# Kernel optimization log

Hardware: AMD Instinct MI355X
Metric: run time of the kernel (lower is better)

The kernel has to match this reference:

```python
import jax, jax.numpy as jnp
import numpy as np

H = 8          # num_heads
NUM_SEEDS = 4  # num_seeds (T = T0 + NUM_SEEDS in training/non_trivial)
NEG_INF = float('-inf')


def setup_inputs() -> dict:
    key = jax.random.key(0)
    ks = jax.random.split(key, 9)
    B, T, L, C = 4, 16, 64, 512
    T0 = T - NUM_SEEDS
    x = jax.random.normal(ks[0], (B, T0 * L, C), dtype=jnp.float32)
    x_ctx = jax.random.normal(ks[1], (B, T, L, C), dtype=jnp.float32)
    dx_ctx = jax.random.normal(ks[2], (B, T, L, C), dtype=jnp.float32)
    ctx_mask = jax.random.randint(ks[3], (B, T), 0, 2).astype(jnp.bool_)
    s = 1.0 / np.sqrt(C)
    qkv_w = jax.random.normal(ks[4], (3 * C, C), dtype=jnp.float32) * s
    k_w = jax.random.normal(ks[5], (C, C), dtype=jnp.float32) * s
    v_w = jax.random.normal(ks[6], (C, C), dtype=jnp.float32) * s
    proj_w = jax.random.normal(ks[7], (C, C), dtype=jnp.float32) * s
    proj_b = jax.random.normal(ks[8], (C,), dtype=jnp.float32) * 0.01
    return {"x": x, "x_ctx": x_ctx, "dx_ctx": dx_ctx, "ctx_mask": ctx_mask,
            "qkv_w": qkv_w, "k_w": k_w, "v_w": v_w, "proj_w": proj_w,
            "proj_b": proj_b}


def reference(x, x_ctx, dx_ctx, ctx_mask, qkv_w, k_w, v_w, proj_w, proj_b):
    B, T, L, C = x_ctx.shape
    T0 = x.shape[1] // L
    hd = C // H
    scale = hd ** (-0.5)

    # qkv for the current (self) tokens: [3, B, H, T0*L, hd]
    qkv = (x @ qkv_w.T).reshape(B, T0 * L, 3, H, hd).transpose(2, 0, 3, 1, 4)
    q, k, v = qkv[0], qkv[1], qkv[2]

    # context keys/values: [B, H, T*L, hd]
    k_ctx = (dx_ctx.reshape(B, T * L, C) @ k_w.T).reshape(B, T * L, H, hd).transpose(0, 2, 1, 3)
    v_ctx = (x_ctx.reshape(B, T * L, C) @ v_w.T).reshape(B, T * L, H, hd).transpose(0, 2, 1, 3)

    # cross-context scores: [B, H, T0*L, T, L]
    attn = (jnp.einsum('bhqd,bhkd->bhqk', q, k_ctx) * scale).reshape(B, H, T0 * L, T, L)

    # context mask: drop whole context frames where ctx_mask is False
    attn = jnp.where(ctx_mask[:, None, None, :, None], attn, NEG_INF)

    # non-trivial temporal mask (training): query frame i can't attend to
    # context frame i + num_seeds
    nt = (jnp.arange(T0)[:, None] + NUM_SEEDS) == jnp.arange(T)[None, :]  # [T0, T]
    attn6 = attn.reshape(B, H, T0, L, T, L)
    attn6 = jnp.where(nt[None, None, :, None, :, None], NEG_INF, attn6)
    attn = attn6.reshape(B, H, T0 * L, T, L)

    # per-frame self attention scores: [B, H, T0, L, L] -> [B, H, T0*L, 1, L]
    q6 = q.reshape(B, H, T0, L, hd)
    k6 = k.reshape(B, H, T0, L, hd)
    self_attn = (jnp.einsum('bhtqd,bhtkd->bhtqk', q6, k6) * scale).reshape(B, H, T0 * L, 1, L)

    # joint softmax over (T+1)*L keys
    attn = jnp.concatenate([attn, self_attn], axis=-2).reshape(B, H, T0 * L, (T + 1) * L)
    attn = jax.nn.softmax(attn, axis=-1)

    # split back: cross part @ v_ctx, self part @ v (per frame)
    out = jnp.einsum('bhqk,bhkd->bhqd', attn[:, :, :, :-L], v_ctx)
    a_self = attn[:, :, :, -L:].reshape(B, H, T0, L, L)
    v6 = v.reshape(B, H, T0, L, hd)
    out = out + jnp.einsum('bhtqk,bhtkd->bhtqd', a_self, v6).reshape(B, H, T0 * L, hd)

    out = out.transpose(0, 2, 1, 3).reshape(B, T0 * L, C)
    return out @ proj_w.T + proj_b
```

## Files before the change

### kernel.cpp

```cpp
#include <hip/hip_runtime.h>
#include <hip/hip_bf16.h>

typedef __attribute__((ext_vector_type(8))) short bf16x8;
typedef __attribute__((ext_vector_type(4))) float f32x4;

#define BB 4
#define TT 16
#define NT0 12
#define LL 64
#define CC 512
#define HH 8
#define HD 64
#define NQ (NT0*LL)
#define NCTX (TT*LL)

#define GPTR(x) ((__attribute__((address_space(1))) void*)(x))
#define SPTR(x) ((__attribute__((address_space(3))) void*)(x))
#define VMCNT(n) (((n) & 15) | (7u << 4) | (0xFu << 8))

__device__ __forceinline__ float bf2f(ushort u) {
  union { unsigned int i; float f; } x; x.i = ((unsigned int)u) << 16; return x.f;
}
__device__ __forceinline__ ushort f2bf(float f) {
  union { float f; unsigned int i; } x; x.f = f;
  unsigned int r = x.i + 0x7fffu + ((x.i >> 16) & 1u);
  return (ushort)(r >> 16);
}

__global__ __launch_bounds__(256) void cvt_all(const float* __restrict__ w0,
                                               const float* __restrict__ w1,
                                               const float* __restrict__ w2,
                                               const float* __restrict__ w3,
                                               const float* __restrict__ x,
                                               const float* __restrict__ xc,
                                               const float* __restrict__ dxc,
                                               ushort* __restrict__ dst) {
  long i = (long)blockIdx.x * 256 + threadIdx.x;
  const float* src; long off;
  if (i < 196608)       { src = w0;  off = 0; }
  else if (i < 262144)  { src = w1;  off = 196608; }
  else if (i < 327680)  { src = w2;  off = 262144; }
  else if (i < 393216)  { src = w3;  off = 327680; }
  else if (i < 786432)  { src = x;   off = 393216; }
  else if (i < 1310720) { src = xc;  off = 786432; }
  else                  { src = dxc; off = 1310720; }
  f32x4 v = *(const f32x4*)(src + (i - off) * 4);
  ushort4 o = { f2bf(v[0]), f2bf(v[1]), f2bf(v[2]), f2bf(v[3]) };
  *(ushort4*)(dst + i * 4) = o;
}

template<int MT>
__device__ __forceinline__ void gemm_mac(const ushort* __restrict__ A,
                                         const ushort* __restrict__ W,
                                         int mt, int nt, ushort* lds,
                                         f32x4* acc) {
  constexpr int ASZ = MT * 32;
  constexpr int BUF = ASZ + 4096;
  constexpr int L   = (MT == 128) ? 4 : 3;

  int t = threadIdx.x;
  int pa0 = t, pa1 = t + 256;
  int ra0 = pa0 >> 2, ra1 = pa1 >> 2;
  int ca0 = (pa0 & 3) ^ ((ra0 >> 1) & 3);
  int ca1 = (pa1 & 3) ^ ((ra1 >> 1) & 3);
  const ushort* ga0 = A + (size_t)(mt * MT + ra0) * 512 + ca0 * 8;
  const ushort* ga1 = A + (size_t)(mt * MT + ra1) * 512 + ca1 * 8;
  const ushort* gw0 = W + (size_t)(nt * 128 + ra0) * 512 + ca0 * 8;
  const ushort* gw1 = W + (size_t)(nt * 128 + ra1) * 512 + ca1 * 8;

  int lane = t & 63, l15 = lane & 15, kg = lane >> 4;
  int wv = t >> 6;
  int mh = (wv >> 1) * (MT / 2), nh = (wv & 1) * 64;
  int swz = kg ^ ((l15 >> 1) & 3);
  int faoff = (mh + l15) * 32 + swz * 8;
  int fwoff = (nh + l15) * 32 + swz * 8;

  auto stage = [&](int ks, int bb) {
    int ko = ks * 32;
    __builtin_amdgcn_global_load_lds(GPTR(ga0 + ko), SPTR(lds + bb + pa0 * 8), 16, 0, 0);
    if (MT == 128)
      __builtin_amdgcn_global_load_lds(GPTR(ga1 + ko), SPTR(lds + bb + pa1 * 8), 16, 0, 0);
    __builtin_amdgcn_global_load_lds(GPTR(gw0 + ko), SPTR(lds + bb + ASZ + pa0 * 8), 16, 0, 0);
    __builtin_amdgcn_global_load_lds(GPTR(gw1 + ko), SPTR(lds + bb + ASZ + pa1 * 8), 16, 0, 0);
  };

  stage(0, 0);
  stage(1, BUF);

#pragma unroll
  for (int ks = 0; ks < 16; ++ks) {
    int cur = (ks % 3) * BUF;
    if (ks < 14) {
      stage(ks + 2, ((ks + 2) % 3) * BUF);
      __builtin_amdgcn_s_waitcnt(VMCNT(2 * L));
    } else if (ks == 14) {
      __builtin_amdgcn_s_waitcnt(VMCNT(L));
    } else {
      __builtin_amdgcn_s_waitcnt(VMCNT(0));
    }
    asm volatile("" ::: "memory");
    __builtin_amdgcn_s_barrier();
    asm volatile("" ::: "memory");

    const ushort* fa = lds + cur + faoff;
    const ushort* fw = lds + cur + ASZ + fwoff;
    bf16x8 af[MT / 32], wf[4];
#pragma unroll
    for (int i = 0; i < MT / 32; ++i) af[i] = *(const bf16x8*)(fa + i * 512);
#pragma unroll
    for (int i = 0; i < 4; ++i) wf[i] = *(const bf16x8*)(fw + i * 512);
#pragma unroll
    for (int mi = 0; mi < MT / 32; ++mi)
#pragma unroll
      for (int ni = 0; ni < 4; ++ni)
        acc[mi * 4 + ni] =
            __builtin_amdgcn_mfma_f32_16x16x32_bf16(af[mi], wf[ni], acc[mi * 4 + ni], 0, 0, 0);

    asm volatile("" ::: "memory");
    __builtin_amdgcn_s_barrier();
    asm volatile("" ::: "memory");
  }
}

template<int MT, int OUTMODE>
__device__ __forceinline__ void gemm_body(const ushort* __restrict__ A,
                                          const ushort* __restrict__ W,
                                          ushort* __restrict__ C,
                                          ushort* __restrict__ CT,
                                          float* __restrict__ Cf,
                                          const float* __restrict__ bias,
                                          int mt, int nt, int N, long TM,
                                          ushort* lds) {
  f32x4 acc[(MT / 32) * 4];
#pragma unroll
  for (int i = 0; i < (MT / 32) * 4; ++i) acc[i] = (f32x4){0, 0, 0, 0};
  gemm_mac<MT>(A, W, mt, nt, lds, acc);

  int lane = threadIdx.x & 63, l15 = lane & 15, kg = lane >> 4;
  int wv = threadIdx.x >> 6;
  int Rw = mt * MT + (wv >> 1) * (MT / 2);
  int Cw = nt * 128 + (wv & 1) * 64;
#pragma unroll
  for (int mi = 0; mi < MT / 32; ++mi) {
    int row = Rw + mi * 16 + kg * 4;
#pragma unroll
    for (int ni = 0; ni < 4; ++ni) {
      f32x4 v = acc[mi * 4 + ni];
      int col = Cw + ni * 16 + l15;
      if (OUTMODE == 0) {
#pragma unroll
        for (int r = 0; r < 4; ++r) C[(size_t)(row + r) * N + col] = f2bf(v[r]);
      } else if (OUTMODE == 1) {
        ushort4 o = { f2bf(v[0]), f2bf(v[1]), f2bf(v[2]), f2bf(v[3]) };
        *(ushort4*)(CT + (long)col * TM + row) = o;
      } else {
        float bv = bias[col];
#pragma unroll
        for (int r = 0; r < 4; ++r) Cf[(size_t)(row + r) * N + col] = v[r] + bv;
      }
    }
  }
}

__global__ __launch_bounds__(256) void gemm3(const ushort* __restrict__ xb,
                                             const ushort* __restrict__ dxb,
                                             const ushort* __restrict__ xcb,
                                             const ushort* __restrict__ qkvwb,
                                             const ushort* __restrict__ kwb,
                                             const ushort* __restrict__ vwb,
                                             ushort* __restrict__ qkv,
                                             ushort* __restrict__ vselfT,
                                             ushort* __restrict__ kctx,
                                             ushort* __restrict__ vctxT) {
  __shared__ ushort lds[24576];
  int blk = blockIdx.x;
  if (blk < 288) {
    int mt = blk % 24, nt = blk / 24;
    if (nt < 8)
      gemm_body<128, 0>(xb, qkvwb, qkv, nullptr, nullptr, nullptr, mt, nt, 1536, 0, lds);
    else
      gemm_body<128, 1>(xb, qkvwb, nullptr, vselfT - (size_t)1024 * 3072, nullptr, nullptr,
                        mt, nt, 1536, 3072, lds);
  } else if (blk < 416) {
    int r = blk - 288;
    gemm_body<128, 0>(dxb, kwb, kctx, nullptr, nullptr, nullptr, r % 32, r / 32, 512, 0, lds);
  } else {
    int r = blk - 416;
    gemm_body<128, 1>(xcb, vwb, nullptr, vctxT, nullptr, nullptr, r % 32, r / 32, 512, 4096, lds);
  }
}

__global__ __launch_bounds__(256) void gemm_proj(const ushort* __restrict__ aout,
                                                 const ushort* __restrict__ pwb,
                                                 const float* __restrict__ bias,
                                                 float* __restrict__ out) {
  __shared__ ushort lds[18432];
  int blk = blockIdx.x;
  gemm_body<64, 2>(aout, pwb, nullptr, nullptr, out, bias, blk % 48, blk / 48, 512, 0, lds);
}

__device__ __forceinline__ void attn_tile32(const ushort* __restrict__ kbase, int kstr,
                                            const ushort* __restrict__ vtb, int vtN,
                                            bf16x8 qa0, bf16x8 qa1,
                                            bf16x8 qb0, bf16x8 qb1,
                                            int l15, int kg,
                                            ushort* __restrict__ Pt,
                                            f32x4 (*acc)[4], float* Lacc) {
  f32x4 s[2][4];
#pragma unroll
  for (int st = 0; st < 4; ++st) {
    const ushort* kp = kbase + (size_t)(st * 16 + l15) * kstr + kg * 8;
    bf16x8 k0 = *(const bf16x8*)kp;
    bf16x8 k1 = *(const bf16x8*)(kp + 32);
    f32x4 z0 = {0, 0, 0, 0}, z1 = {0, 0, 0, 0};
    z0 = __builtin_amdgcn_mfma_f32_16x16x32_bf16(k0, qa0, z0, 0, 0, 0);
    z0 = __builtin_amdgcn_mfma_f32_16x16x32_bf16(k1, qa1, z0, 0, 0, 0);
    z1 = __builtin_amdgcn_mfma_f32_16x16x32_bf16(k0, qb0, z1, 0, 0, 0);
    z1 = __builtin_amdgcn_mfma_f32_16x16x32_bf16(k1, qb1, z1, 0, 0, 0);
    s[0][st] = z0;
    s[1][st] = z1;
  }
#pragma unroll
  for (int qf = 0; qf < 2; ++qf) {
#pragma unroll
    for (int st = 0; st < 4; ++st) {
      float p0 = __builtin_exp2f(fmaf(s[qf][st][0], 0.18033688f, -23.0831206f));
      float p1 = __builtin_exp2f(fmaf(s[qf][st][1], 0.18033688f, -23.0831206f));
      float p2 = __builtin_exp2f(fmaf(s[qf][st][2], 0.18033688f, -23.0831206f));
      float p3 = __builtin_exp2f(fmaf(s[qf][st][3], 0.18033688f, -23.0831206f));
      Lacc[qf] += (p0 + p1) + (p2 + p3);
      ushort4 pk = { f2bf(p0), f2bf(p1), f2bf(p2), f2bf(p3) };
      *(ushort4*)(Pt + qf * 1152 + l15 * 72 + st * 16 + kg * 4) = pk;
    }
  }
#pragma unroll
  for (int kc = 0; kc < 2; ++kc) {
    bf16x8 pb0 = *(const bf16x8*)(Pt + l15 * 72 + kc * 32 + kg * 8);
    bf16x8 pb1 = *(const bf16x8*)(Pt + 1152 + l15 * 72 + kc * 32 + kg * 8);
#pragma unroll
    for (int d = 0; d < 4; ++d) {
      const ushort* vp = vtb + (size_t)(d * 16 + l15) * vtN + kc * 32 + kg * 8;
      bf16x8 vf = *(const bf16x8*)vp;
      acc[0][d] = __builtin_amdgcn_mfma_f32_16x16x32_bf16(vf, pb0, acc[0][d], 0, 0, 0);
      acc[1][d] = __builtin_amdgcn_mfma_f32_16x16x32_bf16(vf, pb1, acc[1][d], 0, 0, 0);
    }
  }
}

__global__ __launch_bounds__(512, 4) void flash_attn(const ushort* __restrict__ qkv,
                                                     const ushort* __restrict__ kctx,
                                                     const ushort* __restrict__ vctxT,
                                                     const ushort* __restrict__ vselfT,
                                                     const int* __restrict__ ctx_mask,
                                                     ushort* __restrict__ aout) {
  __shared__ float smem[13056];
  int blk = blockIdx.x;
  int t0 = blk % NT0;
  int h  = (blk / NT0) % HH;
  int b  = blk / (NT0 * HH);
  int tid = threadIdx.x, wv = tid >> 6, lane = tid & 63;
  int qg = wv >> 2, ks = wv & 3;
  int l15 = lane & 15, kg = lane >> 4;

  int qbase = b * NQ + t0 * LL + qg * 32;
  const ushort* qp0 = qkv + (size_t)(qbase + l15) * 1536 + h * HD + kg * 8;
  const ushort* qp1 = qkv + (size_t)(qbase + 16 + l15) * 1536 + h * HD + kg * 8;
  bf16x8 qa0 = *(const bf16x8*)qp0;
  bf16x8 qa1 = *(const bf16x8*)(qp0 + 32);
  bf16x8 qb0 = *(const bf16x8*)qp1;
  bf16x8 qb1 = *(const bf16x8*)(qp1 + 32);

  f32x4 acc[2][4];
#pragma unroll
  for (int qf = 0; qf < 2; ++qf)
#pragma unroll
    for (int d = 0; d < 4; ++d) acc[qf][d] = (f32x4){0, 0, 0, 0};
  float Lacc[2] = {0.f, 0.f};
  ushort* Pt = (ushort*)smem + wv * 2304;

  int kts[4]; int nkt = 0;
#pragma unroll
  for (int ki = 0; ki < 4; ++ki) {
    int kt = ks * 4 + ki;
    if (ctx_mask[b * TT + kt] != 0 && kt != t0 + 4) kts[nkt++] = kt;
  }

  const ushort* vctxb = vctxT + (size_t)h * HD * (BB * NCTX) + b * NCTX;
  for (int ki = 0; ki < nkt; ++ki) {
    int kt = kts[ki];
    attn_tile32(kctx + (size_t)(b * NCTX + kt * LL) * CC + h * HD, CC,
                vctxb + kt * LL, BB * NCTX,
                qa0, qa1, qb0, qb1, l15, kg, Pt, acc, Lacc);
  }
  if (ks == 0) {
    attn_tile32(qkv + (size_t)(b * NQ + t0 * LL) * 1536 + CC + h * HD, 1536,
                vselfT + (size_t)h * HD * (BB * NQ) + b * NQ + t0 * LL, BB * NQ,
                qa0, qa1, qb0, qb1, l15, kg, Pt, acc, Lacc);
  }

  float L0 = Lacc[0], L1 = Lacc[1];
  L0 += __shfl_xor(L0, 16, 64); L0 += __shfl_xor(L0, 32, 64);
  L1 += __shfl_xor(L1, 16, 64); L1 += __shfl_xor(L1, 32, 64);

  __syncthreads();
  if (ks) {
    float* reg = smem + (size_t)(qg * 3 + ks - 1) * 2176;
#pragma unroll
    for (int qf = 0; qf < 2; ++qf)
#pragma unroll
      for (int d = 0; d < 4; ++d)
        *(f32x4*)(reg + (qf * 64 + lane) * 16 + d * 4) = acc[qf][d];
    reg[2048 + lane * 2]     = L0;
    reg[2048 + lane * 2 + 1] = L1;
  }
  __syncthreads();
  if (!ks) {
    float Ls[2] = {L0, L1};
    f32x4 o[2][4];
#pragma unroll
    for (int qf = 0; qf < 2; ++qf)
#pragma unroll
      for (int d = 0; d < 4; ++d) o[qf][d] = acc[qf][d];
#pragma unroll
    for (int j = 0; j < 3; ++j) {
      const float* reg = smem + (size_t)(qg * 3 + j) * 2176;
      Ls[0] += reg[2048 + lane * 2];
      Ls[1] += reg[2048 + lane * 2 + 1];
#pragma unroll
      for (int qf = 0; qf < 2; ++qf)
#pragma unroll
        for (int d = 0; d < 4; ++d)
          o[qf][d] += *(const f32x4*)(reg + (qf * 64 + lane) * 16 + d * 4);
    }
#pragma unroll
    for (int qf = 0; qf < 2; ++qf) {
      float inv = 1.f / Ls[qf];
      int orow = qbase + qf * 16 + l15;
#pragma unroll
      for (int d = 0; d < 4; ++d) {
        ushort4 ov = { f2bf(o[qf][d][0] * inv), f2bf(o[qf][d][1] * inv),
                       f2bf(o[qf][d][2] * inv), f2bf(o[qf][d][3] * inv) };
        *(ushort4*)(aout + (size_t)orow * CC + h * HD + d * 16 + kg * 4) = ov;
      }
    }
  }
}

extern "C" void kernel_launch(void* const* d_in, const int* in_sizes, int n_in,
                              void* d_out, int out_size, void* d_ws, size_t ws_size,
                              hipStream_t stream) {
  const float* x        = (const float*)d_in[0];
  const float* x_ctx    = (const float*)d_in[1];
  const float* dx_ctx   = (const float*)d_in[2];
  const int*   ctx_mask = (const int*)d_in[3];
  const float* qkv_w    = (const float*)d_in[4];
  const float* k_w      = (const float*)d_in[5];
  const float* v_w      = (const float*)d_in[6];
  const float* proj_w   = (const float*)d_in[7];
  const float* proj_b   = (const float*)d_in[8];
  float* out = (float*)d_out;

  ushort* ws = (ushort*)d_ws;
  ushort* qkvwb  = ws;
  ushort* kwb    = ws + 786432;
  ushort* vwb    = ws + 1048576;
  ushort* pwb    = ws + 1310720;
  ushort* xb     = ws + 1572864;
  ushort* xcb    = ws + 3145728;
  ushort* dxb    = ws + 5242880;
  ushort* qkv    = ws + 7340032;
  ushort* kctx   = ws + 12058624;
  ushort* vctxT  = ws + 14155776;
  ushort* vselfT = ws + 16252928;
  ushort* aout   = ws + 17825792;

  cvt_all<<<7168, 256, 0, stream>>>(qkv_w, k_w, v_w, proj_w, x, x_ctx, dx_ctx, ws);
  gemm3<<<544, 256, 0, stream>>>(xb, dxb, xcb, qkvwb, kwb, vwb,
                                 qkv, vselfT, kctx, vctxT);
  flash_attn<<<384, 512, 0, stream>>>(qkv, kctx, vctxT, vselfT, ctx_mask, aout);
  gemm_proj<<<192, 256, 0, stream>>>(aout, pwb, proj_b, out);
}
```

Before: 139.7 us.

## Skip masked context frames in conversion and GEMMs; widen attention waves to 64 queries

The conversion kernel and the K/V context projections now read ctx_mask and skip work for context frames that are masked out. Those frames are never attended to, so the skip is valid for any mask. The attention kernel is restructured so each 64-lane wave handles all 64 query rows of a frame, with 4 waves per block splitting the key frames. This replaces 8 waves each covering 32 rows, and halves redundant K/V loads per block at the cost of more registers per thread. The risk is lower occupancy and reduced latency hiding in the attention kernel.

```diff
diff --git a/kernel.cpp b/kernel.cpp
--- a/kernel.cpp
+++ b/kernel.cpp
@@ -34,6 +34,7 @@
                                                const float* __restrict__ x,
                                                const float* __restrict__ xc,
                                                const float* __restrict__ dxc,
+                                               const int* __restrict__ ctx_mask,
                                                ushort* __restrict__ dst) {
   long i = (long)blockIdx.x * 256 + threadIdx.x;
   const float* src; long off;
@@ -42,8 +43,15 @@
   else if (i < 327680)  { src = w2;  off = 262144; }
   else if (i < 393216)  { src = w3;  off = 327680; }
   else if (i < 786432)  { src = x;   off = 393216; }
-  else if (i < 1310720) { src = xc;  off = 786432; }
-  else                  { src = dxc; off = 1310720; }
+  else if (i < 1310720) {
+    int r = (int)((i - 786432) >> 7);
+    if (ctx_mask[(r >> 10) * TT + ((r >> 6) & 15)] == 0) return;
+    src = xc;  off = 786432;
+  } else {
+    int r = (int)((i - 1310720) >> 7);
+    if (ctx_mask[(r >> 10) * TT + ((r >> 6) & 15)] == 0) return;
+    src = dxc; off = 1310720;
+  }
   f32x4 v = *(const f32x4*)(src + (i - off) * 4);
   ushort4 o = { f2bf(v[0]), f2bf(v[1]), f2bf(v[2]), f2bf(v[3]) };
   *(ushort4*)(dst + i * 4) = o;
@@ -168,6 +176,7 @@
                                              const ushort* __restrict__ qkvwb,
                                              const ushort* __restrict__ kwb,
                                              const ushort* __restrict__ vwb,
+                                             const int* __restrict__ ctx_mask,
                                              ushort* __restrict__ qkv,
                                              ushort* __restrict__ vselfT,
                                              ushort* __restrict__ kctx,
@@ -183,10 +192,16 @@
                         mt, nt, 1536, 3072, lds);
   } else if (blk < 416) {
     int r = blk - 288;
-    gemm_body<128, 0>(dxb, kwb, kctx, nullptr, nullptr, nullptr, r % 32, r / 32, 512, 0, lds);
+    int mt = r % 32, nt = r / 32;
+    int bb = mt >> 3, f0 = (mt & 7) << 1;
+    if (ctx_mask[bb * TT + f0] == 0 && ctx_mask[bb * TT + f0 + 1] == 0) return;
+    gemm_body<128, 0>(dxb, kwb, kctx, nullptr, nullptr, nullptr, mt, nt, 512, 0, lds);
   } else {
     int r = blk - 416;
-    gemm_body<128, 1>(xcb, vwb, nullptr, vctxT, nullptr, nullptr, r % 32, r / 32, 512, 4096, lds);
+    int mt = r % 32, nt = r / 32;
+    int bb = mt >> 3, f0 = (mt & 7) << 1;
+    if (ctx_mask[bb * TT + f0] == 0 && ctx_mask[bb * TT + f0 + 1] == 0) return;
+    gemm_body<128, 1>(xcb, vwb, nullptr, vctxT, nullptr, nullptr, mt, nt, 512, 4096, lds);
   }
 }
 
@@ -199,35 +214,31 @@
   gemm_body<64, 2>(aout, pwb, nullptr, nullptr, out, bias, blk % 48, blk / 48, 512, 0, lds);
 }
 
-__device__ __forceinline__ void attn_tile32(const ushort* __restrict__ kbase, int kstr,
+__device__ __forceinline__ void attn_tile64(const ushort* __restrict__ kbase, int kstr,
                                             const ushort* __restrict__ vtb, int vtN,
-                                            bf16x8 qa0, bf16x8 qa1,
-                                            bf16x8 qb0, bf16x8 qb1,
+                                            const bf16x8* q0, const bf16x8* q1,
                                             int l15, int kg,
                                             ushort* __restrict__ Pt,
                                             f32x4 (*acc)[4], float* Lacc) {
-  f32x4 s[2][4];
 #pragma unroll
   for (int st = 0; st < 4; ++st) {
     const ushort* kp = kbase + (size_t)(st * 16 + l15) * kstr + kg * 8;
     bf16x8 k0 = *(const bf16x8*)kp;
     bf16x8 k1 = *(const bf16x8*)(kp + 32);
-    f32x4 z0 = {0, 0, 0, 0}, z1 = {0, 0, 0, 0};
-    z0 = __builtin_amdgcn_mfma_f32_16x16x32_bf16(k0, qa0, z0, 0, 0, 0);
-    z0 = __builtin_amdgcn_mfma_f32_16x16x32_bf16(k1, qa1, z0, 0, 0, 0);
-    z1 = __builtin_amdgcn_mfma_f32_16x16x32_bf16(k0, qb0, z1, 0, 0, 0);
-    z1 = __builtin_amdgcn_mfma_f32_16x16x32_bf16(k1, qb1, z1, 0, 0, 0);
-    s[0][st] = z0;
-    s[1][st] = z1;
-  }
-#pragma unroll
-  for (int qf = 0; qf < 2; ++qf) {
-#pragma unroll
-    for (int st = 0; st < 4; ++st) {
-      float p0 = __builtin_exp2f(fmaf(s[qf][st][0], 0.18033688f, -23.0831206f));
-      float p1 = __builtin_exp2f(fmaf(s[qf][st][1], 0.18033688f, -23.0831206f));
-      float p2 = __builtin_exp2f(fmaf(s[qf][st][2], 0.18033688f, -23.0831206f));
-      float p3 = __builtin_exp2f(fmaf(s[qf][st][3], 0.18033688f, -23.0831206f));
+    f32x4 z[4];
+#pragma unroll
+    for (int qf = 0; qf < 4; ++qf) {
+      f32x4 t = {0, 0, 0, 0};
+      t = __builtin_amdgcn_mfma_f32_16x16x32_bf16(k0, q0[qf], t, 0, 0, 0);
+      t = __builtin_amdgcn_mfma_f32_16x16x32_bf16(k1, q1[qf], t, 0, 0, 0);
+      z[qf] = t;
+    }
+#pragma unroll
+    for (int qf = 0; qf < 4; ++qf) {
+      float p0 = __builtin_exp2f(fmaf(z[qf][0], 0.18033688f, -23.0831206f));
+      float p1 = __builtin_exp2f(fmaf(z[qf][1], 0.18033688f, -23.0831206f));
+      float p2 = __builtin_exp2f(fmaf(z[qf][2], 0.18033688f, -23.0831206f));
+      float p3 = __builtin_exp2f(fmaf(z[qf][3], 0.18033688f, -23.0831206f));
       Lacc[qf] += (p0 + p1) + (p2 + p3);
       ushort4 pk = { f2bf(p0), f2bf(p1), f2bf(p2), f2bf(p3) };
       *(ushort4*)(Pt + qf * 1152 + l15 * 72 + st * 16 + kg * 4) = pk;
@@ -235,48 +246,51 @@
   }
 #pragma unroll
   for (int kc = 0; kc < 2; ++kc) {
-    bf16x8 pb0 = *(const bf16x8*)(Pt + l15 * 72 + kc * 32 + kg * 8);
-    bf16x8 pb1 = *(const bf16x8*)(Pt + 1152 + l15 * 72 + kc * 32 + kg * 8);
+    bf16x8 pb[4];
+#pragma unroll
+    for (int qf = 0; qf < 4; ++qf)
+      pb[qf] = *(const bf16x8*)(Pt + qf * 1152 + l15 * 72 + kc * 32 + kg * 8);
 #pragma unroll
     for (int d = 0; d < 4; ++d) {
       const ushort* vp = vtb + (size_t)(d * 16 + l15) * vtN + kc * 32 + kg * 8;
       bf16x8 vf = *(const bf16x8*)vp;
-      acc[0][d] = __builtin_amdgcn_mfma_f32_16x16x32_bf16(vf, pb0, acc[0][d], 0, 0, 0);
-      acc[1][d] = __builtin_amdgcn_mfma_f32_16x16x32_bf16(vf, pb1, acc[1][d], 0, 0, 0);
-    }
-  }
-}
-
-__global__ __launch_bounds__(512, 4) void flash_attn(const ushort* __restrict__ qkv,
-                                                     const ushort* __restrict__ kctx,
-                                                     const ushort* __restrict__ vctxT,
-                                                     const ushort* __restrict__ vselfT,
-                                                     const int* __restrict__ ctx_mask,
-                                                     ushort* __restrict__ aout) {
+#pragma unroll
+      for (int qf = 0; qf < 4; ++qf)
+        acc[qf][d] = __builtin_amdgcn_mfma_f32_16x16x32_bf16(vf, pb[qf], acc[qf][d], 0, 0, 0);
+    }
+  }
+}
+
+__global__ __launch_bounds__(256) void flash_attn(const ushort* __restrict__ qkv,
+                                                  const ushort* __restrict__ kctx,
+                                                  const ushort* __restrict__ vctxT,
+                                                  const ushort* __restrict__ vselfT,
+                                                  const int* __restrict__ ctx_mask,
+                                                  ushort* __restrict__ aout) {
   __shared__ float smem[13056];
   int blk = blockIdx.x;
   int t0 = blk % NT0;
   int h  = (blk / NT0) % HH;
   int b  = blk / (NT0 * HH);
-  int tid = threadIdx.x, wv = tid >> 6, lane = tid & 63;
-  int qg = wv >> 2, ks = wv & 3;
+  int tid = threadIdx.x, ks = tid >> 6, lane = tid & 63;
   int l15 = lane & 15, kg = lane >> 4;
 
-  int qbase = b * NQ + t0 * LL + qg * 32;
-  const ushort* qp0 = qkv + (size_t)(qbase + l15) * 1536 + h * HD + kg * 8;
-  const ushort* qp1 = qkv + (size_t)(qbase + 16 + l15) * 1536 + h * HD + kg * 8;
-  bf16x8 qa0 = *(const bf16x8*)qp0;
-  bf16x8 qa1 = *(const bf16x8*)(qp0 + 32);
-  bf16x8 qb0 = *(const bf16x8*)qp1;
-  bf16x8 qb1 = *(const bf16x8*)(qp1 + 32);
-
-  f32x4 acc[2][4];
-#pragma unroll
-  for (int qf = 0; qf < 2; ++qf)
+  int qbase = b * NQ + t0 * LL;
+  bf16x8 q0[4], q1[4];
+#pragma unroll
+  for (int qf = 0; qf < 4; ++qf) {
+    const ushort* qp = qkv + (size_t)(qbase + qf * 16 + l15) * 1536 + h * HD + kg * 8;
+    q0[qf] = *(const bf16x8*)qp;
+    q1[qf] = *(const bf16x8*)(qp + 32);
+  }
+
+  f32x4 acc[4][4];
+#pragma unroll
+  for (int qf = 0; qf < 4; ++qf)
 #pragma unroll
     for (int d = 0; d < 4; ++d) acc[qf][d] = (f32x4){0, 0, 0, 0};
-  float Lacc[2] = {0.f, 0.f};
-  ushort* Pt = (ushort*)smem + wv * 2304;
+  float Lacc[4] = {0.f, 0.f, 0.f, 0.f};
+  ushort* Pt = (ushort*)smem + ks * 4608;
 
   int kts[4]; int nkt = 0;
 #pragma unroll
@@ -288,58 +302,57 @@
   const ushort* vctxb = vctxT + (size_t)h * HD * (BB * NCTX) + b * NCTX;
   for (int ki = 0; ki < nkt; ++ki) {
     int kt = kts[ki];
-    attn_tile32(kctx + (size_t)(b * NCTX + kt * LL) * CC + h * HD, CC,
+    attn_tile64(kctx + (size_t)(b * NCTX + kt * LL) * CC + h * HD, CC,
                 vctxb + kt * LL, BB * NCTX,
-                qa0, qa1, qb0, qb1, l15, kg, Pt, acc, Lacc);
+                q0, q1, l15, kg, Pt, acc, Lacc);
   }
   if (ks == 0) {
-    attn_tile32(qkv + (size_t)(b * NQ + t0 * LL) * 1536 + CC + h * HD, 1536,
+    attn_tile64(qkv + (size_t)(b * NQ + t0 * LL) * 1536 + CC + h * HD, 1536,
                 vselfT + (size_t)h * HD * (BB * NQ) + b * NQ + t0 * LL, BB * NQ,
-                qa0, qa1, qb0, qb1, l15, kg, Pt, acc, Lacc);
-  }
-
-  float L0 = Lacc[0], L1 = Lacc[1];
-  L0 += __shfl_xor(L0, 16, 64); L0 += __shfl_xor(L0, 32, 64);
-  L1 += __shfl_xor(L1, 16, 64); L1 += __shfl_xor(L1, 32, 64);
+                q0, q1, l15, kg, Pt, acc, Lacc);
+  }
+
+  float L[4];
+#pragma unroll
+  for (int qf = 0; qf < 4; ++qf) {
+    float v = Lacc[qf];
+    v += __shfl_xor(v, 16, 64);
+    v += __shfl_xor(v, 32, 64);
+    L[qf] = v;
+  }
 
   __syncthreads();
   if (ks) {
-    float* reg = smem + (size_t)(qg * 3 + ks - 1) * 2176;
-#pragma unroll
-    for (int qf = 0; qf < 2; ++qf)
+    float* reg = smem + (size_t)(ks - 1) * 4352;
+#pragma unroll
+    for (int qf = 0; qf < 4; ++qf)
 #pragma unroll
       for (int d = 0; d < 4; ++d)
         *(f32x4*)(reg + (qf * 64 + lane) * 16 + d * 4) = acc[qf][d];
-    reg[2048 + lane * 2]     = L0;
-    reg[2048 + lane * 2 + 1] = L1;
+#pragma unroll
+    for (int qf = 0; qf < 4; ++qf) reg[4096 + qf * 64 + lane] = L[qf];
   }
   __syncthreads();
   if (!ks) {
-    float Ls[2] = {L0, L1};
-    f32x4 o[2][4];
-#pragma unroll
-    for (int qf = 0; qf < 2; ++qf)
-#pragma unroll
-      for (int d = 0; d < 4; ++d) o[qf][d] = acc[qf][d];
 #pragma unroll
     for (int j = 0; j < 3; ++j) {
-      const float* reg = smem + (size_t)(qg * 3 + j) * 2176;
-      Ls[0] += reg[2048 + lane * 2];
-      Ls[1] += reg[2048 + lane * 2 + 1];
-#pragma unroll
-      for (int qf = 0; qf < 2; ++qf)
+      const float* reg = smem + (size_t)j * 4352;
+#pragma unroll
+      for (int qf = 0; qf < 4; ++qf) {
+        L[qf] += reg[4096 + qf * 64 + lane];
 #pragma unroll
         for (int d = 0; d < 4; ++d)
-          o[qf][d] += *(const f32x4*)(reg + (qf * 64 + lane) * 16 + d * 4);
-    }
-#pragma unroll
-    for (int qf = 0; qf < 2; ++qf) {
-      float inv = 1.f / Ls[qf];
+          acc[qf][d] += *(const f32x4*)(reg + (qf * 64 + lane) * 16 + d * 4);
+      }
+    }
+#pragma unroll
+    for (int qf = 0; qf < 4; ++qf) {
+      float inv = 1.f / L[qf];
       int orow = qbase + qf * 16 + l15;
 #pragma unroll
       for (int d = 0; d < 4; ++d) {
-        ushort4 ov = { f2bf(o[qf][d][0] * inv), f2bf(o[qf][d][1] * inv),
-                       f2bf(o[qf][d][2] * inv), f2bf(o[qf][d][3] * inv) };
+        ushort4 ov = { f2bf(acc[qf][d][0] * inv), f2bf(acc[qf][d][1] * inv),
+                       f2bf(acc[qf][d][2] * inv), f2bf(acc[qf][d][3] * inv) };
         *(ushort4*)(aout + (size_t)orow * CC + h * HD + d * 16 + kg * 4) = ov;
       }
     }
@@ -374,9 +387,10 @@
   ushort* vselfT = ws + 16252928;
   ushort* aout   = ws + 17825792;
 
-  cvt_all<<<7168, 256, 0, stream>>>(qkv_w, k_w, v_w, proj_w, x, x_ctx, dx_ctx, ws);
-  gemm3<<<544, 256, 0, stream>>>(xb, dxb, xcb, qkvwb, kwb, vwb,
+  cvt_all<<<7168, 256, 0, stream>>>(qkv_w, k_w, v_w, proj_w, x, x_ctx, dx_ctx,
+                                    ctx_mask, ws);
+  gemm3<<<544, 256, 0, stream>>>(xb, dxb, xcb, qkvwb, kwb, vwb, ctx_mask,
                                  qkv, vselfT, kctx, vctxT);
-  flash_attn<<<384, 512, 0, stream>>>(qkv, kctx, vctxT, vselfT, ctx_mask, aout);
+  flash_attn<<<384, 256, 0, stream>>>(qkv, kctx, vctxT, vselfT, ctx_mask, aout);
   gemm_proj<<<192, 256, 0, stream>>>(aout, pwb, proj_b, out);
 }
```

Result: slower. 147.5 us (+5.6%).
